# Performance work log

Hardware: AMD Instinct MI355X
Metric: run time of the kernel (lower is better)

The kernel has to match this reference:

```python
import jax, jax.numpy as jnp
import numpy as np

IN_FEATURES, OUT_FEATURES, KERNEL_DIMS = 1024, 128, 8
BATCH = 256


def setup_inputs() -> dict:
    key = jax.random.key(0)
    kx, kT = jax.random.split(key)
    x = jax.random.normal(kx, (BATCH, IN_FEATURES), dtype=jnp.float32)
    T = jax.random.normal(kT, (IN_FEATURES, OUT_FEATURES, KERNEL_DIMS), dtype=jnp.float32)
    return {"x": x, "T": T}


def reference(x, T):
    B = x.shape[0]
    in_f, out_f, kd = T.shape
    # M: (B, out_features, kernel_dims)
    M = (x @ T.reshape(in_f, out_f * kd)).reshape(B, out_f, kd)
    # pairwise L1 distance over kernel dims: (B, B, out_features)
    diffs = jnp.abs(M[None, :, :, :] - M[:, None, :, :]).sum(axis=3)
    # similarity features: sum over other samples, subtract self-term (exp(0)=1)
    c = jnp.exp(-diffs).sum(axis=1) - 1.0  # (B, out_features)
    return jnp.concatenate([x, c], axis=1)
```

## Files before the change

kernel.cpp:

```cpp
#include <hip/hip_runtime.h>
#include <stdint.h>

#define BATCH 256
#define INF   1024
#define OUTF  128
#define KD    8
#define NN    1024
#define OROW  1152

#define MLS   12
#define CHB   16384
#define NBUF  8
#define TP8   1056

typedef __attribute__((ext_vector_type(4))) float f32x4;

__global__ __launch_bounds__(256) void prep_kernel(
    const float* __restrict__ x, const float* __restrict__ T,
    float* __restrict__ out, unsigned char* __restrict__ x8,
    unsigned char* __restrict__ Tt8)
{
    __shared__ unsigned char lds8[64 * 68];
    int bid = blockIdx.x;
    int t = threadIdx.x;
    if (bid < 256) {
        int i0 = (bid >> 4) << 6;
        int n0 = (bid & 15) << 6;
        int tx = t & 63, ty = t >> 6;
        for (int r = ty; r < 64; r += 4) {
            float v = T[(size_t)(i0 + r) * NN + n0 + tx];
            lds8[tx * 68 + r] =
                (unsigned char)(__builtin_amdgcn_cvt_pk_fp8_f32(v, v, 0, false) & 0xff);
        }
        __syncthreads();
        #pragma unroll
        for (int p = 0; p < 4; ++p) {
            int q = p * 1024 + t * 4;
            int n = q >> 6, i = q & 63;
            uint32_t w = *(const uint32_t*)(lds8 + n * 68 + i);
            *(uint32_t*)(Tt8 + (size_t)(n0 + n) * INF + i0 + i) = w;
        }
    } else {
        int bx = bid - 256;
        #pragma unroll
        for (int p = 0; p < 4; ++p) {
            int a = bx * 4 + p;
            int j = t * 4;
            float4 v = *(const float4*)(x + (size_t)a * INF + j);
            *(float4*)(out + (size_t)a * OROW + j) = v;
            uint32_t w = (uint32_t)__builtin_amdgcn_cvt_pk_fp8_f32(v.x, v.y, 0, false);
            w = (uint32_t)__builtin_amdgcn_cvt_pk_fp8_f32(v.z, v.w, (int)w, true);
            *(uint32_t*)(x8 + (size_t)a * INF + j) = w;
        }
    }
}

__device__ __forceinline__ void stage_x8(
    const unsigned char* __restrict__ x8, unsigned char* lbuf,
    int c, int wave, int lane)
{
    const int r16 = lane >> 2;
    const int slot = lane & 3;
    #pragma unroll
    for (int p = 0; p < 2; ++p) {
        const int i = wave * 2 + p;
        const unsigned char* src = x8 + (size_t)(i * 16 + r16) * INF
                                       + c * 64 + ((slot ^ (r16 & 3)) << 4);
        unsigned char* dst = lbuf + i * 1024;
        __builtin_amdgcn_global_load_lds(
            (const __attribute__((address_space(1))) unsigned int*)src,
            (__attribute__((address_space(3))) unsigned int*)dst, 16, 0, 0);
    }
}

#define GEMM_STEP(c, VM) do {                                                 \
    const uint32_t bb = xlsBase + (uint32_t)(((c) & 7) * CHB);                \
    const uint32_t tb = tslBase + oB + (uint32_t)((c) << 6);                  \
    long long A00, A01, A10, A11, B0, B1;                                     \
    asm volatile(                                                             \
        "s_waitcnt vmcnt(" #VM ")\n\t"                                        \
        "ds_read_b64 %0, %6\n\t"                                              \
        "ds_read_b64 %1, %7\n\t"                                              \
        "ds_read_b64 %2, %8\n\t"                                              \
        "ds_read_b64 %3, %9\n\t"                                              \
        "ds_read_b64 %4, %10\n\t"                                             \
        "ds_read_b64 %5, %11\n\t"                                             \
        "s_waitcnt lgkmcnt(0)"                                                \
        : "=v"(A00), "=v"(A01), "=v"(A10), "=v"(A11), "=v"(B0), "=v"(B1)      \
        : "v"(bb + aA00), "v"(bb + aA01), "v"(bb + aA00 + 1024),              \
          "v"(bb + aA01 + 1024), "v"(tb), "v"(tb + 32)                        \
        : "memory");                                                          \
    acc0 = __builtin_amdgcn_mfma_f32_16x16x32_fp8_fp8(A00, B0, acc0, 0, 0, 0);\
    acc0 = __builtin_amdgcn_mfma_f32_16x16x32_fp8_fp8(A01, B1, acc0, 0, 0, 0);\
    acc1 = __builtin_amdgcn_mfma_f32_16x16x32_fp8_fp8(A10, B0, acc1, 0, 0, 0);\
    acc1 = __builtin_amdgcn_mfma_f32_16x16x32_fp8_fp8(A11, B1, acc1, 0, 0, 0);\
} while (0)

__global__ __launch_bounds__(512, 1) void fused_kernel(
    const unsigned char* __restrict__ x8, const unsigned char* __restrict__ Tt8,
    float* __restrict__ out)
{
    __shared__ __align__(16) unsigned char xls[NBUF * CHB];
    __shared__ __align__(16) union {
        unsigned char Tsl[8 * TP8];
        float red[512];
    } u;
    __shared__ __align__(16) float Mloc[256 * MLS];

    const int o = blockIdx.x >> 1;
    const int half = blockIdx.x & 1;
    const int t = threadIdx.x;
    const int wave = t >> 6, lane = t & 63;

    {
        const unsigned char* src = Tt8 + (size_t)(o * 8 + wave) * INF + lane * 16;
        unsigned char* dst = u.Tsl + wave * TP8;
        __builtin_amdgcn_global_load_lds(
            (const __attribute__((address_space(1))) unsigned int*)src,
            (__attribute__((address_space(3))) unsigned int*)dst, 16, 0, 0);
    }
    #pragma unroll
    for (int c = 0; c < 7; ++c)
        stage_x8(x8, xls + c * CHB, c, wave, lane);
    __syncthreads();

    const int rc = lane & 15, quad = lane >> 4;
    const int abase = wave * 32;
    f32x4 acc0 = {0.f, 0.f, 0.f, 0.f}, acc1 = {0.f, 0.f, 0.f, 0.f};

    const uint32_t xlsBase = (uint32_t)(uintptr_t)(&xls[0]);
    const uint32_t tslBase = (uint32_t)(uintptr_t)(&u.Tsl[0]);
    const uint32_t rowOff = (uint32_t)((abase + rc) * 64);
    const uint32_t aA00 = rowOff
        + (uint32_t)(((((quad >> 1)) ^ (rc & 3)) << 4) + (quad & 1) * 8);
    const uint32_t aA01 = rowOff
        + (uint32_t)((((2 + (quad >> 1)) ^ (rc & 3)) << 4) + (quad & 1) * 8);
    const uint32_t oB = (uint32_t)((rc & 7) * TP8 + quad * 8);

    for (int c = 0; c < 9; ++c) {
        stage_x8(x8, xls + ((c + 7) & 7) * CHB, c + 7, wave, lane);
        GEMM_STEP(c, 14);
    }
    GEMM_STEP(9, 12);
    GEMM_STEP(10, 10);
    GEMM_STEP(11, 8);
    GEMM_STEP(12, 6);
    GEMM_STEP(13, 4);
    GEMM_STEP(14, 2);
    GEMM_STEP(15, 0);

    if (rc < 8) {
        #pragma unroll
        for (int r = 0; r < 4; ++r) {
            Mloc[(abase + quad * 4 + r) * MLS + rc]      = acc0[r];
            Mloc[(abase + 16 + quad * 4 + r) * MLS + rc] = acc1[r];
        }
    }
    __syncthreads();

    const int ar = t & 127;
    const int bq = t >> 7;
    const int a = half * 128 + ar;
    f32x4 m0 = *(const f32x4*)(Mloc + a * MLS);
    f32x4 m1 = *(const f32x4*)(Mloc + a * MLS + 4);
    float ssum = 0.f;
    #pragma unroll 4
    for (int j = 0; j < 64; ++j) {
        const float* qp = Mloc + (bq * 64 + j) * MLS;
        f32x4 q0 = *(const f32x4*)(qp);
        f32x4 q1 = *(const f32x4*)(qp + 4);
        float d = fabsf(m0[0] - q0[0]) + fabsf(m0[1] - q0[1])
                + fabsf(m0[2] - q0[2]) + fabsf(m0[3] - q0[3])
                + fabsf(m1[0] - q1[0]) + fabsf(m1[1] - q1[1])
                + fabsf(m1[2] - q1[2]) + fabsf(m1[3] - q1[3]);
        ssum += __expf(-d);
    }
    u.red[t] = ssum;
    __syncthreads();
    if (t < 128) {
        float s = u.red[t] + u.red[t + 128] + u.red[t + 256] + u.red[t + 384];
        out[(size_t)(half * 128 + t) * OROW + INF + o] = s - 1.0f;
    }
}

extern "C" void kernel_launch(void* const* d_in, const int* in_sizes, int n_in,
                              void* d_out, int out_size, void* d_ws, size_t ws_size,
                              hipStream_t stream) {
    const float* x = (const float*)d_in[0];
    const float* T = (const float*)d_in[1];
    float* out = (float*)d_out;
    unsigned char* x8  = (unsigned char*)d_ws;
    unsigned char* Tt8 = (unsigned char*)d_ws + 262144;

    prep_kernel<<<320, 256, 0, stream>>>(x, T, out, x8, Tt8);
    fused_kernel<<<256, 512, 0, stream>>>(x8, Tt8, out);
}
```

Baseline: 72.79 us.

## Double fused kernel block to 1024 threads, one 16-row tile per wave

Launches the fused GEMM+similarity kernel with 16 waves instead of 8. Each wave now handles a single 16-row MFMA tile instead of two, with even and odd k-halves accumulated separately and summed at the end. Staging becomes one async load per wave per chunk, and wait counts are adjusted to match. The pairwise loop is split 8 ways instead of 4. The aim is more latency hiding and shorter per-thread work, at the cost of more waves per block and a larger reduction.

```diff
diff --git a/kernel.cpp b/kernel.cpp
--- a/kernel.cpp
+++ b/kernel.cpp
@@ -55,55 +55,46 @@
     }
 }
 
-__device__ __forceinline__ void stage_x8(
+__device__ __forceinline__ void stage1(
     const unsigned char* __restrict__ x8, unsigned char* lbuf,
     int c, int wave, int lane)
 {
     const int r16 = lane >> 2;
     const int slot = lane & 3;
-    #pragma unroll
-    for (int p = 0; p < 2; ++p) {
-        const int i = wave * 2 + p;
-        const unsigned char* src = x8 + (size_t)(i * 16 + r16) * INF
-                                       + c * 64 + ((slot ^ (r16 & 3)) << 4);
-        unsigned char* dst = lbuf + i * 1024;
-        __builtin_amdgcn_global_load_lds(
-            (const __attribute__((address_space(1))) unsigned int*)src,
-            (__attribute__((address_space(3))) unsigned int*)dst, 16, 0, 0);
-    }
+    const unsigned char* src = x8 + (size_t)(wave * 16 + r16) * INF
+                                   + c * 64 + ((slot ^ (r16 & 3)) << 4);
+    unsigned char* dst = lbuf + wave * 1024;
+    __builtin_amdgcn_global_load_lds(
+        (const __attribute__((address_space(1))) unsigned int*)src,
+        (__attribute__((address_space(3))) unsigned int*)dst, 16, 0, 0);
 }
 
 #define GEMM_STEP(c, VM) do {                                                 \
     const uint32_t bb = xlsBase + (uint32_t)(((c) & 7) * CHB);                \
     const uint32_t tb = tslBase + oB + (uint32_t)((c) << 6);                  \
-    long long A00, A01, A10, A11, B0, B1;                                     \
+    long long A00, A01, B0, B1;                                               \
     asm volatile(                                                             \
         "s_waitcnt vmcnt(" #VM ")\n\t"                                        \
-        "ds_read_b64 %0, %6\n\t"                                              \
-        "ds_read_b64 %1, %7\n\t"                                              \
-        "ds_read_b64 %2, %8\n\t"                                              \
-        "ds_read_b64 %3, %9\n\t"                                              \
-        "ds_read_b64 %4, %10\n\t"                                             \
-        "ds_read_b64 %5, %11\n\t"                                             \
+        "ds_read_b64 %0, %4\n\t"                                              \
+        "ds_read_b64 %1, %5\n\t"                                              \
+        "ds_read_b64 %2, %6\n\t"                                              \
+        "ds_read_b64 %3, %7\n\t"                                              \
         "s_waitcnt lgkmcnt(0)"                                                \
-        : "=v"(A00), "=v"(A01), "=v"(A10), "=v"(A11), "=v"(B0), "=v"(B1)      \
-        : "v"(bb + aA00), "v"(bb + aA01), "v"(bb + aA00 + 1024),              \
-          "v"(bb + aA01 + 1024), "v"(tb), "v"(tb + 32)                        \
+        : "=v"(A00), "=v"(A01), "=v"(B0), "=v"(B1)                            \
+        : "v"(bb + aA00), "v"(bb + aA01), "v"(tb), "v"(tb + 32)               \
         : "memory");                                                          \
-    acc0 = __builtin_amdgcn_mfma_f32_16x16x32_fp8_fp8(A00, B0, acc0, 0, 0, 0);\
-    acc0 = __builtin_amdgcn_mfma_f32_16x16x32_fp8_fp8(A01, B1, acc0, 0, 0, 0);\
-    acc1 = __builtin_amdgcn_mfma_f32_16x16x32_fp8_fp8(A10, B0, acc1, 0, 0, 0);\
-    acc1 = __builtin_amdgcn_mfma_f32_16x16x32_fp8_fp8(A11, B1, acc1, 0, 0, 0);\
+    accE = __builtin_amdgcn_mfma_f32_16x16x32_fp8_fp8(A00, B0, accE, 0, 0, 0);\
+    accO = __builtin_amdgcn_mfma_f32_16x16x32_fp8_fp8(A01, B1, accO, 0, 0, 0);\
 } while (0)
 
-__global__ __launch_bounds__(512, 1) void fused_kernel(
+__global__ __launch_bounds__(1024, 1) void fused_kernel(
     const unsigned char* __restrict__ x8, const unsigned char* __restrict__ Tt8,
     float* __restrict__ out)
 {
     __shared__ __align__(16) unsigned char xls[NBUF * CHB];
     __shared__ __align__(16) union {
         unsigned char Tsl[8 * TP8];
-        float red[512];
+        float red[1024];
     } u;
     __shared__ __align__(16) float Mloc[256 * MLS];
 
@@ -112,7 +103,7 @@
     const int t = threadIdx.x;
     const int wave = t >> 6, lane = t & 63;
 
-    {
+    if (wave < 8) {
         const unsigned char* src = Tt8 + (size_t)(o * 8 + wave) * INF + lane * 16;
         unsigned char* dst = u.Tsl + wave * TP8;
         __builtin_amdgcn_global_load_lds(
@@ -121,16 +112,15 @@
     }
     #pragma unroll
     for (int c = 0; c < 7; ++c)
-        stage_x8(x8, xls + c * CHB, c, wave, lane);
+        stage1(x8, xls + c * CHB, c, wave, lane);
     __syncthreads();
 
     const int rc = lane & 15, quad = lane >> 4;
-    const int abase = wave * 32;
-    f32x4 acc0 = {0.f, 0.f, 0.f, 0.f}, acc1 = {0.f, 0.f, 0.f, 0.f};
+    f32x4 accE = {0.f, 0.f, 0.f, 0.f}, accO = {0.f, 0.f, 0.f, 0.f};
 
     const uint32_t xlsBase = (uint32_t)(uintptr_t)(&xls[0]);
     const uint32_t tslBase = (uint32_t)(uintptr_t)(&u.Tsl[0]);
-    const uint32_t rowOff = (uint32_t)((abase + rc) * 64);
+    const uint32_t rowOff = (uint32_t)((wave * 16 + rc) * 64);
     const uint32_t aA00 = rowOff
         + (uint32_t)(((((quad >> 1)) ^ (rc & 3)) << 4) + (quad & 1) * 8);
     const uint32_t aA01 = rowOff
@@ -138,23 +128,21 @@
     const uint32_t oB = (uint32_t)((rc & 7) * TP8 + quad * 8);
 
     for (int c = 0; c < 9; ++c) {
-        stage_x8(x8, xls + ((c + 7) & 7) * CHB, c + 7, wave, lane);
-        GEMM_STEP(c, 14);
+        stage1(x8, xls + ((c + 7) & 7) * CHB, c + 7, wave, lane);
+        GEMM_STEP(c, 7);
     }
-    GEMM_STEP(9, 12);
-    GEMM_STEP(10, 10);
-    GEMM_STEP(11, 8);
-    GEMM_STEP(12, 6);
-    GEMM_STEP(13, 4);
-    GEMM_STEP(14, 2);
+    GEMM_STEP(9, 6);
+    GEMM_STEP(10, 5);
+    GEMM_STEP(11, 4);
+    GEMM_STEP(12, 3);
+    GEMM_STEP(13, 2);
+    GEMM_STEP(14, 1);
     GEMM_STEP(15, 0);
 
     if (rc < 8) {
         #pragma unroll
-        for (int r = 0; r < 4; ++r) {
-            Mloc[(abase + quad * 4 + r) * MLS + rc]      = acc0[r];
-            Mloc[(abase + 16 + quad * 4 + r) * MLS + rc] = acc1[r];
-        }
+        for (int r = 0; r < 4; ++r)
+            Mloc[(wave * 16 + quad * 4 + r) * MLS + rc] = accE[r] + accO[r];
     }
     __syncthreads();
 
@@ -165,8 +153,8 @@
     f32x4 m1 = *(const f32x4*)(Mloc + a * MLS + 4);
     float ssum = 0.f;
     #pragma unroll 4
-    for (int j = 0; j < 64; ++j) {
-        const float* qp = Mloc + (bq * 64 + j) * MLS;
+    for (int j = 0; j < 32; ++j) {
+        const float* qp = Mloc + (bq * 32 + j) * MLS;
         f32x4 q0 = *(const f32x4*)(qp);
         f32x4 q1 = *(const f32x4*)(qp + 4);
         float d = fabsf(m0[0] - q0[0]) + fabsf(m0[1] - q0[1])
@@ -178,7 +166,9 @@
     u.red[t] = ssum;
     __syncthreads();
     if (t < 128) {
-        float s = u.red[t] + u.red[t + 128] + u.red[t + 256] + u.red[t + 384];
+        float s = 0.f;
+        #pragma unroll
+        for (int q = 0; q < 8; ++q) s += u.red[t + q * 128];
         out[(size_t)(half * 128 + t) * OROW + INF + o] = s - 1.0f;
     }
 }
@@ -193,5 +183,5 @@
     unsigned char* Tt8 = (unsigned char*)d_ws + 262144;
 
     prep_kernel<<<320, 256, 0, stream>>>(x, T, out, x8, Tt8);
-    fused_kernel<<<256, 512, 0, stream>>>(x8, Tt8, out);
+    fused_kernel<<<256, 1024, 0, stream>>>(x8, Tt8, out);
 }
```

After: 72.67 us. About the same (-0.2%).

## Double chunk size to 128 K-bytes with 4 buffers and split accumulators

Applied to the files above, without the earlier changes.

Restructures the fp8 GEMM pipeline so each staged chunk covers 128 bytes of K per row in a 4-deep ring instead of 64 bytes in an 8-deep ring, halving the number of wait/read/MFMA steps. Each step now issues 12 LDS reads and 8 MFMAs, and the work is spread over four independent accumulators that are summed at the end, which shortens the MFMA dependency chains. The XOR swizzle widens to 8 slots to match the 128-byte rows. The cost is fewer chunks in flight, which may expose more global-load latency, plus higher register pressure.

```diff
diff --git a/kernel.cpp b/kernel.cpp
--- a/kernel.cpp
+++ b/kernel.cpp
@@ -9,8 +9,8 @@
 #define OROW  1152
 
 #define MLS   12
-#define CHB   16384
-#define NBUF  8
+#define CHB   32768
+#define NBUF  4
 #define TP8   1056
 
 typedef __attribute__((ext_vector_type(4))) float f32x4;
@@ -55,18 +55,18 @@
     }
 }
 
-__device__ __forceinline__ void stage_x8(
+__device__ __forceinline__ void stage1(
     const unsigned char* __restrict__ x8, unsigned char* lbuf,
     int c, int wave, int lane)
 {
-    const int r16 = lane >> 2;
-    const int slot = lane & 3;
+    const int rin = lane >> 3;
+    const int slot = lane & 7;
     #pragma unroll
-    for (int p = 0; p < 2; ++p) {
-        const int i = wave * 2 + p;
-        const unsigned char* src = x8 + (size_t)(i * 16 + r16) * INF
-                                       + c * 64 + ((slot ^ (r16 & 3)) << 4);
-        unsigned char* dst = lbuf + i * 1024;
+    for (int p = 0; p < 4; ++p) {
+        const int row = wave * 32 + p * 8 + rin;
+        const unsigned char* src = x8 + (size_t)row * INF
+                                       + c * 128 + ((slot ^ rin) << 4);
+        unsigned char* dst = lbuf + wave * 4096 + p * 1024;
         __builtin_amdgcn_global_load_lds(
             (const __attribute__((address_space(1))) unsigned int*)src,
             (__attribute__((address_space(3))) unsigned int*)dst, 16, 0, 0);
@@ -74,26 +74,40 @@
 }
 
 #define GEMM_STEP(c, VM) do {                                                 \
-    const uint32_t bb = xlsBase + (uint32_t)(((c) & 7) * CHB);                \
-    const uint32_t tb = tslBase + oB + (uint32_t)((c) << 6);                  \
-    long long A00, A01, A10, A11, B0, B1;                                     \
+    const uint32_t bb = xlsBase + (uint32_t)(((c) & 3) * CHB);                \
+    const uint32_t tb = tslBase + oB + (uint32_t)((c) << 7);                  \
+    long long A00, A01, A02, A03, A10, A11, A12, A13, B0, B1, B2, B3;         \
     asm volatile(                                                             \
         "s_waitcnt vmcnt(" #VM ")\n\t"                                        \
-        "ds_read_b64 %0, %6\n\t"                                              \
-        "ds_read_b64 %1, %7\n\t"                                              \
-        "ds_read_b64 %2, %8\n\t"                                              \
-        "ds_read_b64 %3, %9\n\t"                                              \
-        "ds_read_b64 %4, %10\n\t"                                             \
-        "ds_read_b64 %5, %11\n\t"                                             \
+        "ds_read_b64 %0, %12\n\t"                                             \
+        "ds_read_b64 %1, %13\n\t"                                             \
+        "ds_read_b64 %2, %14\n\t"                                             \
+        "ds_read_b64 %3, %15\n\t"                                             \
+        "ds_read_b64 %4, %16\n\t"                                             \
+        "ds_read_b64 %5, %17\n\t"                                             \
+        "ds_read_b64 %6, %18\n\t"                                             \
+        "ds_read_b64 %7, %19\n\t"                                             \
+        "ds_read_b64 %8, %20\n\t"                                             \
+        "ds_read_b64 %9, %21\n\t"                                             \
+        "ds_read_b64 %10, %22\n\t"                                            \
+        "ds_read_b64 %11, %23\n\t"                                            \
         "s_waitcnt lgkmcnt(0)"                                                \
-        : "=v"(A00), "=v"(A01), "=v"(A10), "=v"(A11), "=v"(B0), "=v"(B1)      \
-        : "v"(bb + aA00), "v"(bb + aA01), "v"(bb + aA00 + 1024),              \
-          "v"(bb + aA01 + 1024), "v"(tb), "v"(tb + 32)                        \
+        : "=&v"(A00), "=&v"(A01), "=&v"(A02), "=&v"(A03),                     \
+          "=&v"(A10), "=&v"(A11), "=&v"(A12), "=&v"(A13),                     \
+          "=&v"(B0), "=&v"(B1), "=&v"(B2), "=&v"(B3)                          \
+        : "v"(bb + aL0), "v"(bb + aL1), "v"(bb + aL2), "v"(bb + aL3),         \
+          "v"(bb + aL0 + 2048), "v"(bb + aL1 + 2048),                         \
+          "v"(bb + aL2 + 2048), "v"(bb + aL3 + 2048),                         \
+          "v"(tb), "v"(tb + 32), "v"(tb + 64), "v"(tb + 96)                   \
         : "memory");                                                          \
-    acc0 = __builtin_amdgcn_mfma_f32_16x16x32_fp8_fp8(A00, B0, acc0, 0, 0, 0);\
-    acc0 = __builtin_amdgcn_mfma_f32_16x16x32_fp8_fp8(A01, B1, acc0, 0, 0, 0);\
-    acc1 = __builtin_amdgcn_mfma_f32_16x16x32_fp8_fp8(A10, B0, acc1, 0, 0, 0);\
-    acc1 = __builtin_amdgcn_mfma_f32_16x16x32_fp8_fp8(A11, B1, acc1, 0, 0, 0);\
+    accL0 = __builtin_amdgcn_mfma_f32_16x16x32_fp8_fp8(A00, B0, accL0, 0, 0, 0);\
+    accH0 = __builtin_amdgcn_mfma_f32_16x16x32_fp8_fp8(A10, B0, accH0, 0, 0, 0);\
+    accL1 = __builtin_amdgcn_mfma_f32_16x16x32_fp8_fp8(A01, B1, accL1, 0, 0, 0);\
+    accH1 = __builtin_amdgcn_mfma_f32_16x16x32_fp8_fp8(A11, B1, accH1, 0, 0, 0);\
+    accL0 = __builtin_amdgcn_mfma_f32_16x16x32_fp8_fp8(A02, B2, accL0, 0, 0, 0);\
+    accH0 = __builtin_amdgcn_mfma_f32_16x16x32_fp8_fp8(A12, B2, accH0, 0, 0, 0);\
+    accL1 = __builtin_amdgcn_mfma_f32_16x16x32_fp8_fp8(A03, B3, accL1, 0, 0, 0);\
+    accH1 = __builtin_amdgcn_mfma_f32_16x16x32_fp8_fp8(A13, B3, accH1, 0, 0, 0);\
 } while (0)
 
 __global__ __launch_bounds__(512, 1) void fused_kernel(
@@ -119,41 +133,39 @@
             (const __attribute__((address_space(1))) unsigned int*)src,
             (__attribute__((address_space(3))) unsigned int*)dst, 16, 0, 0);
     }
-    #pragma unroll
-    for (int c = 0; c < 7; ++c)
-        stage_x8(x8, xls + c * CHB, c, wave, lane);
+    stage1(x8, xls + 0 * CHB, 0, wave, lane);
+    stage1(x8, xls + 1 * CHB, 1, wave, lane);
+    stage1(x8, xls + 2 * CHB, 2, wave, lane);
     __syncthreads();
 
     const int rc = lane & 15, quad = lane >> 4;
     const int abase = wave * 32;
-    f32x4 acc0 = {0.f, 0.f, 0.f, 0.f}, acc1 = {0.f, 0.f, 0.f, 0.f};
+    f32x4 accL0 = {0.f,0.f,0.f,0.f}, accL1 = {0.f,0.f,0.f,0.f};
+    f32x4 accH0 = {0.f,0.f,0.f,0.f}, accH1 = {0.f,0.f,0.f,0.f};
 
     const uint32_t xlsBase = (uint32_t)(uintptr_t)(&xls[0]);
     const uint32_t tslBase = (uint32_t)(uintptr_t)(&u.Tsl[0]);
-    const uint32_t rowOff = (uint32_t)((abase + rc) * 64);
-    const uint32_t aA00 = rowOff
-        + (uint32_t)(((((quad >> 1)) ^ (rc & 3)) << 4) + (quad & 1) * 8);
-    const uint32_t aA01 = rowOff
-        + (uint32_t)((((2 + (quad >> 1)) ^ (rc & 3)) << 4) + (quad & 1) * 8);
+    const uint32_t rowOff = (uint32_t)((abase + rc) * 128);
+    const uint32_t qlo = (uint32_t)((quad & 1) * 8);
+    const uint32_t aL0 = rowOff + ((((0u * 2 + (quad >> 1)) ^ (rc & 7)) << 4) + qlo);
+    const uint32_t aL1 = rowOff + ((((1u * 2 + (quad >> 1)) ^ (rc & 7)) << 4) + qlo);
+    const uint32_t aL2 = rowOff + ((((2u * 2 + (quad >> 1)) ^ (rc & 7)) << 4) + qlo);
+    const uint32_t aL3 = rowOff + ((((3u * 2 + (quad >> 1)) ^ (rc & 7)) << 4) + qlo);
     const uint32_t oB = (uint32_t)((rc & 7) * TP8 + quad * 8);
 
-    for (int c = 0; c < 9; ++c) {
-        stage_x8(x8, xls + ((c + 7) & 7) * CHB, c + 7, wave, lane);
-        GEMM_STEP(c, 14);
-    }
-    GEMM_STEP(9, 12);
-    GEMM_STEP(10, 10);
-    GEMM_STEP(11, 8);
-    GEMM_STEP(12, 6);
-    GEMM_STEP(13, 4);
-    GEMM_STEP(14, 2);
-    GEMM_STEP(15, 0);
+    for (int c = 0; c < 5; ++c) {
+        stage1(x8, xls + ((c + 3) & 3) * CHB, c + 3, wave, lane);
+        GEMM_STEP(c, 12);
+    }
+    GEMM_STEP(5, 8);
+    GEMM_STEP(6, 4);
+    GEMM_STEP(7, 0);
 
     if (rc < 8) {
         #pragma unroll
         for (int r = 0; r < 4; ++r) {
-            Mloc[(abase + quad * 4 + r) * MLS + rc]      = acc0[r];
-            Mloc[(abase + 16 + quad * 4 + r) * MLS + rc] = acc1[r];
+            Mloc[(abase + quad * 4 + r) * MLS + rc]      = accL0[r] + accL1[r];
+            Mloc[(abase + 16 + quad * 4 + r) * MLS + rc] = accH0[r] + accH1[r];
         }
     }
     __syncthreads();
```

After: 72.11 us. No clear change (-0.9%).
